# Performance work log

Measured on AMD Instinct MI355X. Metric: run time of the kernel, lower is better.

The kernel has to match this reference:

```python
import jax, jax.numpy as jnp
import numpy as np

RES = 512
N_LAYERS = 3
BATCH = 128
NUM_CLASSES = 10
LAMBDA = 5.32e-07
K = 2.0 * np.pi / LAMBDA  # module-level constant k in the original code
Z = 0.035                 # propagation distance d
DX = 1e-06                # pixel pitch


def _transfer_function(res):
    # Angular-spectrum Fresnel transfer function H(fx, fy), static numpy precompute.
    fx = np.fft.fftfreq(res, DX)
    FX, FY = np.meshgrid(fx, fx)
    H = np.exp(1j * K * Z) * np.exp(-1j * np.pi * LAMBDA * Z * (FX ** 2 + FY ** 2))
    return jnp.asarray(H.astype(np.complex64))


def setup_inputs() -> dict:
    key = jax.random.key(0)
    k1, k2, k3, k4 = jax.random.split(key, 4)
    x = jax.random.normal(k1, (BATCH, 1, RES, RES), dtype=jnp.float32)
    phases = jax.random.normal(k2, (N_LAYERS, RES, RES), dtype=jnp.float32) * 0.1
    fc_w = jax.random.normal(k3, (NUM_CLASSES, RES * RES), dtype=jnp.float32) * 0.01
    fc_b = jax.random.normal(k4, (NUM_CLASSES,), dtype=jnp.float32) * 0.01
    return {"x": x, "phases": phases, "fc_w": fc_w, "fc_b": fc_b}


def reference(x, phases, fc_w, fc_b):
    res = x.shape[-1]
    H = _transfer_function(res)  # (res, res) complex64
    field = x[:, 0].astype(jnp.complex64)  # (B, res, res)
    for i in range(phases.shape[0]):
        # phase-mask multiply, then Fresnel propagation: ifft2(fft2(field) * H)
        field = field * jnp.exp(1j * phases[i])
        field = jnp.fft.ifft2(jnp.fft.fft2(field, axes=(-2, -1)) * H, axes=(-2, -1))
    intensity = field.real ** 2 + field.imag ** 2  # |field|^2
    feat = intensity.reshape(x.shape[0], -1)
    return feat @ fc_w.T + fc_b
```

## Files before the change

kernel.cpp:

```cpp
#include <hip/hip_runtime.h>
#include <math.h>


#define PAD(i) ((i) + ((i) >> 4))
#define LSTR 545
#define PSTR 545

typedef __attribute__((ext_vector_type(2))) _Float16 half2v;
typedef __attribute__((ext_vector_type(8))) _Float16 half8;

__device__ __forceinline__ void wave_lds_order() {
  asm volatile("" ::: "memory");
}

__device__ __forceinline__ float2 cadd(float2 a, float2 b){ return make_float2(a.x+b.x, a.y+b.y); }
__device__ __forceinline__ float2 csub(float2 a, float2 b){ return make_float2(a.x-b.x, a.y-b.y); }
__device__ __forceinline__ float2 cmul(float2 a, float2 b){ return make_float2(a.x*b.x - a.y*b.y, a.x*b.y + a.y*b.x); }

template<int S>
__device__ __forceinline__ float2 cmul_s(float2 a, float2 b) {
  return (S < 0) ? make_float2(a.x*b.x - a.y*b.y, a.x*b.y + a.y*b.x)
                 : make_float2(a.x*b.x + a.y*b.y, a.y*b.x - a.x*b.y);
}

template<int S>
__device__ __forceinline__ float2 crot(float2 z){
  return (S > 0) ? make_float2(-z.y, z.x) : make_float2(z.y, -z.x);
}

template<int S>
__device__ __forceinline__ void fft8(float2 v[8]) {
  const float sq = 0.70710678118654752440f;
  float2 t0 = cadd(v[0], v[4]), t1 = csub(v[0], v[4]);
  float2 t2 = cadd(v[2], v[6]), t3 = csub(v[2], v[6]);
  float2 E0 = cadd(t0, t2), E2 = csub(t0, t2);
  float2 rt3 = crot<S>(t3);
  float2 E1 = cadd(t1, rt3), E3 = csub(t1, rt3);
  float2 u0 = cadd(v[1], v[5]), u1 = csub(v[1], v[5]);
  float2 u2 = cadd(v[3], v[7]), u3 = csub(v[3], v[7]);
  float2 O0 = cadd(u0, u2), O2 = csub(u0, u2);
  float2 ru3 = crot<S>(u3);
  float2 O1 = cadd(u1, ru3), O3 = csub(u1, ru3);
  float2 O1w = make_float2(sq*(O1.x - (float)S*O1.y), sq*((float)S*O1.x + O1.y));
  float2 O2w = crot<S>(O2);
  float2 O3w = make_float2(-sq*(O3.x + (float)S*O3.y), sq*((float)S*O3.x - O3.y));
  v[0] = cadd(E0, O0);  v[4] = csub(E0, O0);
  v[1] = cadd(E1, O1w); v[5] = csub(E1, O1w);
  v[2] = cadd(E2, O2w); v[6] = csub(E2, O2w);
  v[3] = cadd(E3, O3w); v[7] = csub(E3, O3w);
}

__device__ __forceinline__ void mktw(float2 tw2[7], float2 tw3[7], int t) {
  float a2 = -6.28318530717958647692f * (float)(t & 7) / 64.0f;
  float a3 = -6.28318530717958647692f * (float)(t & 63) / 512.0f;
  float s2, c2; __sincosf(a2, &s2, &c2);
  float s3, c3; __sincosf(a3, &s3, &c3);
  float2 w2 = make_float2(c2, s2), w3 = make_float2(c3, s3);
  tw2[0] = w2; tw3[0] = w3;
  #pragma unroll
  for (int r = 1; r < 7; ++r) { tw2[r] = cmul(tw2[r-1], w2); tw3[r] = cmul(tw3[r-1], w3); }
}

template<int S>
__device__ __forceinline__ void fft512_w(float2 v[8], float2* __restrict__ B, int t,
                                         const float2 tw2[7], const float2 tw3[7]) {
  fft8<S>(v);
  #pragma unroll
  for (int r = 0; r < 8; ++r) B[PAD(8*t + r)] = v[r];
  wave_lds_order();
  #pragma unroll
  for (int r = 0; r < 8; ++r) v[r] = B[PAD(t + 64*r)];
  #pragma unroll
  for (int r = 1; r < 8; ++r) v[r] = cmul_s<S>(v[r], tw2[r-1]);
  fft8<S>(v);
  int d = ((t >> 3) << 6) | (t & 7);
  #pragma unroll
  for (int r = 0; r < 8; ++r) B[PAD(d + 8*r)] = v[r];
  wave_lds_order();
  #pragma unroll
  for (int r = 0; r < 8; ++r) v[r] = B[PAD(t + 64*r)];
  #pragma unroll
  for (int r = 1; r < 8; ++r) v[r] = cmul_s<S>(v[r], tw3[r-1]);
  fft8<S>(v);
}

template<int S>
__device__ __forceinline__ void fft512_pair(float2 vA[8], float2 vB[8],
                                            float4* __restrict__ B, int t,
                                            const float2 tw2[7], const float2 tw3[7]) {
  fft8<S>(vA); fft8<S>(vB);
  #pragma unroll
  for (int r = 0; r < 8; ++r)
    B[PAD(8*t + r)] = make_float4(vA[r].x, vA[r].y, vB[r].x, vB[r].y);
  wave_lds_order();
  #pragma unroll
  for (int r = 0; r < 8; ++r) {
    float4 w = B[PAD(t + 64*r)];
    vA[r] = make_float2(w.x, w.y); vB[r] = make_float2(w.z, w.w);
  }
  #pragma unroll
  for (int r = 1; r < 8; ++r) {
    vA[r] = cmul_s<S>(vA[r], tw2[r-1]); vB[r] = cmul_s<S>(vB[r], tw2[r-1]);
  }
  fft8<S>(vA); fft8<S>(vB);
  int d = ((t >> 3) << 6) | (t & 7);
  #pragma unroll
  for (int r = 0; r < 8; ++r)
    B[PAD(d + 8*r)] = make_float4(vA[r].x, vA[r].y, vB[r].x, vB[r].y);
  wave_lds_order();
  #pragma unroll
  for (int r = 0; r < 8; ++r) {
    float4 w = B[PAD(t + 64*r)];
    vA[r] = make_float2(w.x, w.y); vB[r] = make_float2(w.z, w.w);
  }
  #pragma unroll
  for (int r = 1; r < 8; ++r) {
    vA[r] = cmul_s<S>(vA[r], tw3[r-1]); vB[r] = cmul_s<S>(vB[r], tw3[r-1]);
  }
  fft8<S>(vA); fft8<S>(vB);
}

__device__ __forceinline__ float2 h2f(half2v h) { return make_float2((float)h[0], (float)h[1]); }
__device__ __forceinline__ half2v f2h(float2 v) { half2v h; h[0] = (_Float16)v.x; h[1] = (_Float16)v.y; return h; }


__global__ __launch_bounds__(256) void k_hinit(float2* __restrict__ hx,
                                               float2* __restrict__ hy) {
  int idx = blockIdx.x * 256 + threadIdx.x;
  int u = idx & 511;
  double f = (double)(u < 256 ? u : u - 512) * 1953.125;
  const double LAM = 5.32e-7, ZD = 0.035;
  const double PI = 3.14159265358979323846;
  double s, c;
  if (idx < 512) {
    double ang = -PI * LAM * ZD * f * f;
    sincos(ang, &s, &c);
    hx[u] = make_float2((float)c, (float)s);
  } else {
    double ang = (2.0 * PI / LAM) * ZD - PI * LAM * ZD * f * f;
    sincos(ang, &s, &c);
    const double sc = 1.0 / 262144.0;
    hy[u] = make_float2((float)(c * sc), (float)(s * sc));
  }
}

__global__ __launch_bounds__(256) void k_r1(const float* __restrict__ x,
                                            const float* __restrict__ ph,
                                            half2v* __restrict__ F) {
  __shared__ float2 lds[4 * LSTR];
  int tid = threadIdx.x;
  int t = tid & 63, rl = tid >> 6;
  size_t row = (size_t)blockIdx.x * 4 + rl;
  int y = (int)(row & 511);
  const float* xr = x + row * 512;
  const float* pr = ph + (size_t)y * 512;
  float2 tw2[7], tw3[7];
  mktw(tw2, tw3, t);
  float2 v[8];
  #pragma unroll
  for (int r = 0; r < 8; ++r) {
    int e = t + 64*r;
    float a = xr[e];
    float p = pr[e];
    float sn, cs; __sincosf(p, &sn, &cs);
    v[r] = make_float2(a * cs, a * sn);
  }
  fft512_w<-1>(v, lds + rl * LSTR, t, tw2, tw3);
  half2v* Fr = F + row * 512;
  #pragma unroll
  for (int r = 0; r < 8; ++r) Fr[t + 64*r] = f2h(v[r]);
}

__global__ __launch_bounds__(256) void k_rmid(half2v* __restrict__ F,
                                              const float* __restrict__ ph) {
  __shared__ float2 lds[4 * LSTR];
  int tid = threadIdx.x;
  int t = tid & 63, rl = tid >> 6;
  size_t row = (size_t)blockIdx.x * 4 + rl;
  int y = (int)(row & 511);
  half2v* Fr = F + row * 512;
  const float* pr = ph + (size_t)y * 512;
  float pv[8];
  #pragma unroll
  for (int r = 0; r < 8; ++r) pv[r] = pr[t + 64*r];
  float2 tw2[7], tw3[7];
  mktw(tw2, tw3, t);
  float2 v[8];
  #pragma unroll
  for (int r = 0; r < 8; ++r) v[r] = h2f(Fr[t + 64*r]);
  fft512_w<1>(v, lds + rl * LSTR, t, tw2, tw3);
  #pragma unroll
  for (int r = 0; r < 8; ++r) {
    float sn, cs; __sincosf(pv[r], &sn, &cs);
    v[r] = cmul(v[r], make_float2(cs, sn));
  }
  fft512_w<-1>(v, lds + rl * LSTR, t, tw2, tw3);
  #pragma unroll
  for (int r = 0; r < 8; ++r) Fr[t + 64*r] = f2h(v[r]);
}

__global__ __launch_bounds__(512) void k_col(half2v* __restrict__ F,
                                             const float2* __restrict__ hx,
                                             const float2* __restrict__ hy,
                                             int ntiles) {
  __shared__ float4 lds[8 * PSTR];
  int tid = threadIdx.x;
  int t = tid & 63, cl = tid >> 6;
  float2 hyv[8];
  #pragma unroll
  for (int r = 0; r < 8; ++r) hyv[r] = hy[t + 64*r];
  float2 tw2[7], tw3[7];
  mktw(tw2, tw3, t);

  int tile = blockIdx.x;
  half8 pf[4];
  if (tile < ntiles) {
    int b = tile >> 5, x0 = (tile & 31) << 4;
    const half8* Fb8 = (const half8*)(F + (size_t)b * 262144);
    #pragma unroll
    for (int i = 0; i < 4; ++i) {
      int f = tid + 512 * i;
      int yy = f >> 2, c4 = f & 3;
      pf[i] = Fb8[(size_t)yy * 128 + (x0 >> 2) + c4];
    }
  }
  while (tile < ntiles) {
    int b = tile >> 5, x0 = (tile & 31) << 4;
    half8* Fb8 = (half8*)(F + (size_t)b * 262144);
    float2 hxA = hx[x0 + 2*cl], hxB = hx[x0 + 2*cl + 1];
    #pragma unroll
    for (int i = 0; i < 4; ++i) {
      int f = tid + 512 * i;
      int yy = f >> 2, c4 = f & 3;
      half8 d = pf[i];
      int pb = PAD(yy);
      lds[(2*c4)     * PSTR + pb] = make_float4((float)d[0], (float)d[1],
                                                (float)d[2], (float)d[3]);
      lds[(2*c4 + 1) * PSTR + pb] = make_float4((float)d[4], (float)d[5],
                                                (float)d[6], (float)d[7]);
    }
    int next = tile + (int)gridDim.x;
    if (next < ntiles) {
      int nb = next >> 5, nx0 = (next & 31) << 4;
      const half8* Nb8 = (const half8*)(F + (size_t)nb * 262144);
      #pragma unroll
      for (int i = 0; i < 4; ++i) {
        int f = tid + 512 * i;
        int yy = f >> 2, c4 = f & 3;
        pf[i] = Nb8[(size_t)yy * 128 + (nx0 >> 2) + c4];
      }
    }
    __syncthreads();
    float4* B = lds + cl * PSTR;
    float2 vA[8], vB[8];
    #pragma unroll
    for (int r = 0; r < 8; ++r) {
      float4 w = B[PAD(t + 64*r)];
      vA[r] = make_float2(w.x, w.y); vB[r] = make_float2(w.z, w.w);
    }
    fft512_pair<-1>(vA, vB, B, t, tw2, tw3);
    #pragma unroll
    for (int r = 0; r < 8; ++r) {
      vA[r] = cmul(cmul(vA[r], hyv[r]), hxA);
      vB[r] = cmul(cmul(vB[r], hyv[r]), hxB);
    }
    fft512_pair<1>(vA, vB, B, t, tw2, tw3);
    #pragma unroll
    for (int r = 0; r < 8; ++r)
      B[PAD(t + 64*r)] = make_float4(vA[r].x, vA[r].y, vB[r].x, vB[r].y);
    __syncthreads();
    #pragma unroll
    for (int i = 0; i < 4; ++i) {
      int f = tid + 512 * i;
      int yy = f >> 2, c4 = f & 3;
      int pb = PAD(yy);
      float4 a  = lds[(2*c4)     * PSTR + pb];
      float4 bb = lds[(2*c4 + 1) * PSTR + pb];
      half8 o;
      o[0] = (_Float16)a.x;  o[1] = (_Float16)a.y;
      o[2] = (_Float16)a.z;  o[3] = (_Float16)a.w;
      o[4] = (_Float16)bb.x; o[5] = (_Float16)bb.y;
      o[6] = (_Float16)bb.z; o[7] = (_Float16)bb.w;
      Fb8[(size_t)yy * 128 + (x0 >> 2) + c4] = o;
    }
    __syncthreads();
    tile = next;
  }
}

__global__ __launch_bounds__(256) void k_rlast(const half2v* __restrict__ F,
                                               const float* __restrict__ W,
                                               float* __restrict__ partial, int m) {
  __shared__ float2 lds[4 * LSTR];
  int tid = threadIdx.x;
  int t = tid & 63, rl = tid >> 6;
  int nq = (m + 3) >> 2;
  int y = blockIdx.x / nq;
  int q = blockIdx.x - y * nq;
  int g = q * 4 + rl;
  bool act = (g < m);
  const half2v* Fr = F + ((size_t)g * 262144 + (size_t)y * 512);
  float2 tw2[7], tw3[7];
  mktw(tw2, tw3, t);
  float2 v[8];
  #pragma unroll
  for (int r = 0; r < 8; ++r) {
    half2v h = act ? Fr[t + 64*r] : (half2v)(_Float16)0.0f;
    v[r] = h2f(h);
  }
  fft512_w<1>(v, lds + rl * LSTR, t, tw2, tw3);
  float acc[10];
  #pragma unroll
  for (int c = 0; c < 10; ++c) acc[c] = 0.0f;
  const float* Wy = W + (size_t)y * 512;
  #pragma unroll
  for (int r = 0; r < 8; ++r) {
    int e = t + 64*r;
    float I = v[r].x * v[r].x + v[r].y * v[r].y;
    #pragma unroll
    for (int c = 0; c < 10; ++c) acc[c] += I * Wy[(size_t)c * 262144 + e];
  }
  float mine = 0.0f;
  #pragma unroll
  for (int c = 0; c < 10; ++c) {
    float s = acc[c];
    #pragma unroll
    for (int off = 32; off > 0; off >>= 1) s += __shfl_xor(s, off, 64);
    if (t == c) mine = s;
  }
  if (act && t < 10)
    partial[((size_t)g * 10 + t) * 512 + y] = mine;
}

__global__ __launch_bounds__(64) void k_fc(const float* __restrict__ partial,
                                           const float* __restrict__ fc_b,
                                           float* __restrict__ out, int b0, int m) {
  int bid = blockIdx.x;
  int g = bid / 10, c = bid - g * 10;
  int t = threadIdx.x;
  const float* p = partial + ((size_t)g * 10 + c) * 512;
  float s = 0.0f;
  #pragma unroll
  for (int r = 0; r < 8; ++r) s += p[t + 64*r];
  #pragma unroll
  for (int off = 32; off > 0; off >>= 1) s += __shfl_xor(s, off, 64);
  if (t == 0) out[(size_t)(b0 + g) * 10 + c] = s + fc_b[c];
}


extern "C" void kernel_launch(void* const* d_in, const int* in_sizes, int n_in,
                              void* d_out, int out_size, void* d_ws, size_t ws_size,
                              hipStream_t stream) {
  const float* x    = (const float*)d_in[0];
  const float* ph   = (const float*)d_in[1];
  const float* fc_w = (const float*)d_in[2];
  const float* fc_b = (const float*)d_in[3];
  float* out = (float*)d_out;

  const size_t IMG = 262144;
  const size_t PER_IMG = IMG * sizeof(half2v) + 512 * 10 * sizeof(float);
  float2* hx = (float2*)d_ws;
  float2* hy = hx + 512;
  size_t avail = (ws_size > IMG * sizeof(float2)) ? ws_size - IMG * sizeof(float2) : 0;
  int M = (int)(avail / PER_IMG);
  if (M < 1) M = 1;
  if (M > 128) M = 128;
  half2v* F  = (half2v*)((char*)d_ws + IMG * sizeof(float2));
  float* part = (float*)((char*)F + (size_t)M * IMG * sizeof(half2v));

  hipLaunchKernelGGL(k_hinit, dim3(4), dim3(256), 0, stream, hx, hy);

  for (int b0 = 0; b0 < 128; b0 += M) {
    int m = (128 - b0 < M) ? (128 - b0) : M;
    int rblocks = m * 128;
    int ntiles = m * 32;
    int cgrid = ntiles < 512 ? ntiles : 512;
    int nq = (m + 3) >> 2;
    hipLaunchKernelGGL(k_r1,    dim3(rblocks), dim3(256), 0, stream, x + (size_t)b0 * IMG, ph, F);
    hipLaunchKernelGGL(k_col,   dim3(cgrid), dim3(512), 0, stream, F, (const float2*)hx, (const float2*)hy, ntiles);
    hipLaunchKernelGGL(k_rmid,  dim3(rblocks), dim3(256), 0, stream, F, ph + IMG);
    hipLaunchKernelGGL(k_col,   dim3(cgrid), dim3(512), 0, stream, F, (const float2*)hx, (const float2*)hy, ntiles);
    hipLaunchKernelGGL(k_rmid,  dim3(rblocks), dim3(256), 0, stream, F, ph + 2 * IMG);
    hipLaunchKernelGGL(k_col,   dim3(cgrid), dim3(512), 0, stream, F, (const float2*)hx, (const float2*)hy, ntiles);
    hipLaunchKernelGGL(k_rlast, dim3(512 * nq), dim3(256), 0, stream, F, fc_w, part, m);
    hipLaunchKernelGGL(k_fc,    dim3(m * 10), dim3(64), 0, stream, part, fc_b, out, b0, m);
  }
}
```

Measured before the change: 695.5 us.

## Make row FFT kernels persistent with register prefetch of next row group

```diff
diff --git a/kernel.cpp b/kernel.cpp
--- a/kernel.cpp
+++ b/kernel.cpp
@@ -146,57 +146,86 @@
 
 __global__ __launch_bounds__(256) void k_r1(const float* __restrict__ x,
                                             const float* __restrict__ ph,
-                                            half2v* __restrict__ F) {
+                                            half2v* __restrict__ F, int ng) {
   __shared__ float2 lds[4 * LSTR];
   int tid = threadIdx.x;
   int t = tid & 63, rl = tid >> 6;
-  size_t row = (size_t)blockIdx.x * 4 + rl;
-  int y = (int)(row & 511);
-  const float* xr = x + row * 512;
-  const float* pr = ph + (size_t)y * 512;
   float2 tw2[7], tw3[7];
   mktw(tw2, tw3, t);
-  float2 v[8];
-  #pragma unroll
-  for (int r = 0; r < 8; ++r) {
-    int e = t + 64*r;
-    float a = xr[e];
-    float p = pr[e];
-    float sn, cs; __sincosf(p, &sn, &cs);
-    v[r] = make_float2(a * cs, a * sn);
-  }
-  fft512_w<-1>(v, lds + rl * LSTR, t, tw2, tw3);
-  half2v* Fr = F + row * 512;
-  #pragma unroll
-  for (int r = 0; r < 8; ++r) Fr[t + 64*r] = f2h(v[r]);
+  int grp = blockIdx.x;
+  float pfx[8], pfp[8];
+  if (grp < ng) {
+    size_t row = (size_t)grp * 4 + rl;
+    const float* xr = x + row * 512;
+    const float* pr = ph + (size_t)(row & 511) * 512;
+    #pragma unroll
+    for (int r = 0; r < 8; ++r) { pfx[r] = xr[t + 64*r]; pfp[r] = pr[t + 64*r]; }
+  }
+  while (grp < ng) {
+    size_t row = (size_t)grp * 4 + rl;
+    float2 v[8];
+    #pragma unroll
+    for (int r = 0; r < 8; ++r) {
+      float sn, cs; __sincosf(pfp[r], &sn, &cs);
+      v[r] = make_float2(pfx[r] * cs, pfx[r] * sn);
+    }
+    int next = grp + (int)gridDim.x;
+    if (next < ng) {
+      size_t nrow = (size_t)next * 4 + rl;
+      const float* xr = x + nrow * 512;
+      const float* pr = ph + (size_t)(nrow & 511) * 512;
+      #pragma unroll
+      for (int r = 0; r < 8; ++r) { pfx[r] = xr[t + 64*r]; pfp[r] = pr[t + 64*r]; }
+    }
+    fft512_w<-1>(v, lds + rl * LSTR, t, tw2, tw3);
+    half2v* Fr = F + row * 512;
+    #pragma unroll
+    for (int r = 0; r < 8; ++r) Fr[t + 64*r] = f2h(v[r]);
+    grp = next;
+  }
 }
 
 __global__ __launch_bounds__(256) void k_rmid(half2v* __restrict__ F,
-                                              const float* __restrict__ ph) {
+                                              const float* __restrict__ ph, int ng) {
   __shared__ float2 lds[4 * LSTR];
   int tid = threadIdx.x;
   int t = tid & 63, rl = tid >> 6;
-  size_t row = (size_t)blockIdx.x * 4 + rl;
-  int y = (int)(row & 511);
-  half2v* Fr = F + row * 512;
-  const float* pr = ph + (size_t)y * 512;
-  float pv[8];
-  #pragma unroll
-  for (int r = 0; r < 8; ++r) pv[r] = pr[t + 64*r];
   float2 tw2[7], tw3[7];
   mktw(tw2, tw3, t);
-  float2 v[8];
-  #pragma unroll
-  for (int r = 0; r < 8; ++r) v[r] = h2f(Fr[t + 64*r]);
-  fft512_w<1>(v, lds + rl * LSTR, t, tw2, tw3);
-  #pragma unroll
-  for (int r = 0; r < 8; ++r) {
-    float sn, cs; __sincosf(pv[r], &sn, &cs);
-    v[r] = cmul(v[r], make_float2(cs, sn));
-  }
-  fft512_w<-1>(v, lds + rl * LSTR, t, tw2, tw3);
-  #pragma unroll
-  for (int r = 0; r < 8; ++r) Fr[t + 64*r] = f2h(v[r]);
+  int grp = blockIdx.x;
+  half2v pff[8]; float pfp[8];
+  if (grp < ng) {
+    size_t row = (size_t)grp * 4 + rl;
+    const half2v* Fr = F + row * 512;
+    const float* pr = ph + (size_t)(row & 511) * 512;
+    #pragma unroll
+    for (int r = 0; r < 8; ++r) { pff[r] = Fr[t + 64*r]; pfp[r] = pr[t + 64*r]; }
+  }
+  while (grp < ng) {
+    size_t row = (size_t)grp * 4 + rl;
+    float2 v[8]; float cur_p[8];
+    #pragma unroll
+    for (int r = 0; r < 8; ++r) { v[r] = h2f(pff[r]); cur_p[r] = pfp[r]; }
+    int next = grp + (int)gridDim.x;
+    if (next < ng) {
+      size_t nrow = (size_t)next * 4 + rl;
+      const half2v* Fr = F + nrow * 512;
+      const float* pr = ph + (size_t)(nrow & 511) * 512;
+      #pragma unroll
+      for (int r = 0; r < 8; ++r) { pff[r] = Fr[t + 64*r]; pfp[r] = pr[t + 64*r]; }
+    }
+    fft512_w<1>(v, lds + rl * LSTR, t, tw2, tw3);
+    #pragma unroll
+    for (int r = 0; r < 8; ++r) {
+      float sn, cs; __sincosf(cur_p[r], &sn, &cs);
+      v[r] = cmul(v[r], make_float2(cs, sn));
+    }
+    fft512_w<-1>(v, lds + rl * LSTR, t, tw2, tw3);
+    half2v* Fr = F + row * 512;
+    #pragma unroll
+    for (int r = 0; r < 8; ++r) Fr[t + 64*r] = f2h(v[r]);
+    grp = next;
+  }
 }
 
 __global__ __launch_bounds__(512) void k_col(half2v* __restrict__ F,
@@ -290,46 +319,63 @@
 
 __global__ __launch_bounds__(256) void k_rlast(const half2v* __restrict__ F,
                                                const float* __restrict__ W,
-                                               float* __restrict__ partial, int m) {
+                                               float* __restrict__ partial,
+                                               int m, int nblk) {
   __shared__ float2 lds[4 * LSTR];
   int tid = threadIdx.x;
   int t = tid & 63, rl = tid >> 6;
   int nq = (m + 3) >> 2;
-  int y = blockIdx.x / nq;
-  int q = blockIdx.x - y * nq;
-  int g = q * 4 + rl;
-  bool act = (g < m);
-  const half2v* Fr = F + ((size_t)g * 262144 + (size_t)y * 512);
   float2 tw2[7], tw3[7];
   mktw(tw2, tw3, t);
-  float2 v[8];
-  #pragma unroll
-  for (int r = 0; r < 8; ++r) {
-    half2v h = act ? Fr[t + 64*r] : (half2v)(_Float16)0.0f;
-    v[r] = h2f(h);
-  }
-  fft512_w<1>(v, lds + rl * LSTR, t, tw2, tw3);
-  float acc[10];
-  #pragma unroll
-  for (int c = 0; c < 10; ++c) acc[c] = 0.0f;
-  const float* Wy = W + (size_t)y * 512;
-  #pragma unroll
-  for (int r = 0; r < 8; ++r) {
-    int e = t + 64*r;
-    float I = v[r].x * v[r].x + v[r].y * v[r].y;
-    #pragma unroll
-    for (int c = 0; c < 10; ++c) acc[c] += I * Wy[(size_t)c * 262144 + e];
-  }
-  float mine = 0.0f;
-  #pragma unroll
-  for (int c = 0; c < 10; ++c) {
-    float s = acc[c];
-    #pragma unroll
-    for (int off = 32; off > 0; off >>= 1) s += __shfl_xor(s, off, 64);
-    if (t == c) mine = s;
-  }
-  if (act && t < 10)
-    partial[((size_t)g * 10 + t) * 512 + y] = mine;
+  int bid = blockIdx.x;
+  half2v pff[8];
+  if (bid < nblk) {
+    int y = bid / nq, q = bid - y * nq, g = q * 4 + rl;
+    bool act = (g < m);
+    const half2v* Fr = F + ((size_t)g * 262144 + (size_t)y * 512);
+    #pragma unroll
+    for (int r = 0; r < 8; ++r)
+      pff[r] = act ? Fr[t + 64*r] : (half2v)(_Float16)0.0f;
+  }
+  while (bid < nblk) {
+    int y = bid / nq, q = bid - y * nq, g = q * 4 + rl;
+    bool act = (g < m);
+    float2 v[8];
+    #pragma unroll
+    for (int r = 0; r < 8; ++r) v[r] = h2f(pff[r]);
+    int next = bid + (int)gridDim.x;
+    if (next < nblk) {
+      int ny = next / nq, nqq = next - ny * nq, ng2 = nqq * 4 + rl;
+      bool nact = (ng2 < m);
+      const half2v* Fr = F + ((size_t)ng2 * 262144 + (size_t)ny * 512);
+      #pragma unroll
+      for (int r = 0; r < 8; ++r)
+        pff[r] = nact ? Fr[t + 64*r] : (half2v)(_Float16)0.0f;
+    }
+    fft512_w<1>(v, lds + rl * LSTR, t, tw2, tw3);
+    float acc[10];
+    #pragma unroll
+    for (int c = 0; c < 10; ++c) acc[c] = 0.0f;
+    const float* Wy = W + (size_t)y * 512;
+    #pragma unroll
+    for (int r = 0; r < 8; ++r) {
+      int e = t + 64*r;
+      float I = v[r].x * v[r].x + v[r].y * v[r].y;
+      #pragma unroll
+      for (int c = 0; c < 10; ++c) acc[c] += I * Wy[(size_t)c * 262144 + e];
+    }
+    float mine = 0.0f;
+    #pragma unroll
+    for (int c = 0; c < 10; ++c) {
+      float s = acc[c];
+      #pragma unroll
+      for (int off = 32; off > 0; off >>= 1) s += __shfl_xor(s, off, 64);
+      if (t == c) mine = s;
+    }
+    if (act && t < 10)
+      partial[((size_t)g * 10 + t) * 512 + y] = mine;
+    bid = next;
+  }
 }
 
 __global__ __launch_bounds__(64) void k_fc(const float* __restrict__ partial,
@@ -372,17 +418,20 @@
 
   for (int b0 = 0; b0 < 128; b0 += M) {
     int m = (128 - b0 < M) ? (128 - b0) : M;
-    int rblocks = m * 128;
+    int ng = m * 128;
+    int rgrid = ng < 2048 ? ng : 2048;
     int ntiles = m * 32;
     int cgrid = ntiles < 512 ? ntiles : 512;
     int nq = (m + 3) >> 2;
-    hipLaunchKernelGGL(k_r1,    dim3(rblocks), dim3(256), 0, stream, x + (size_t)b0 * IMG, ph, F);
+    int nblk = 512 * nq;
+    int lgrid = nblk < 2048 ? nblk : 2048;
+    hipLaunchKernelGGL(k_r1,    dim3(rgrid), dim3(256), 0, stream, x + (size_t)b0 * IMG, ph, F, ng);
     hipLaunchKernelGGL(k_col,   dim3(cgrid), dim3(512), 0, stream, F, (const float2*)hx, (const float2*)hy, ntiles);
-    hipLaunchKernelGGL(k_rmid,  dim3(rblocks), dim3(256), 0, stream, F, ph + IMG);
+    hipLaunchKernelGGL(k_rmid,  dim3(rgrid), dim3(256), 0, stream, F, ph + IMG, ng);
     hipLaunchKernelGGL(k_col,   dim3(cgrid), dim3(512), 0, stream, F, (const float2*)hx, (const float2*)hy, ntiles);
-    hipLaunchKernelGGL(k_rmid,  dim3(rblocks), dim3(256), 0, stream, F, ph + 2 * IMG);
+    hipLaunchKernelGGL(k_rmid,  dim3(rgrid), dim3(256), 0, stream, F, ph + 2 * IMG, ng);
     hipLaunchKernelGGL(k_col,   dim3(cgrid), dim3(512), 0, stream, F, (const float2*)hx, (const float2*)hy, ntiles);
-    hipLaunchKernelGGL(k_rlast, dim3(512 * nq), dim3(256), 0, stream, F, fc_w, part, m);
+    hipLaunchKernelGGL(k_rlast, dim3(lgrid), dim3(256), 0, stream, F, fc_w, part, m, nblk);
     hipLaunchKernelGGL(k_fc,    dim3(m * 10), dim3(64), 0, stream, part, fc_b, out, b0, m);
   }
 }
```

Measured after the change: 765.3 us. 10.0% more time.
